# Kernel optimization log

Hardware: AMD Instinct MI355X
Metric: run time of the kernel (lower is better)

## Reference

```python
import jax, jax.numpy as jnp
import numpy as np
import math

H, W = 2048, 2048
Q_QUALITY = 50


def _dct_matrix():
    A = np.zeros((8, 8), dtype=np.float32)
    for i in range(8):
        for j in range(8):
            a = math.sqrt(1 / 8) if i == 0 else math.sqrt(1 / 4)
            A[i, j] = a * math.cos(math.pi * (j + 0.5) * i / 8)
    return A

_A = jnp.array(_dct_matrix())
_Qc = jnp.array([[17,18,24,47,99,99,99,99],[18,21,26,66,99,99,99,99],[24,26,56,99,99,99,99,99],[47,66,99,99,99,99,99,99],[99,99,99,99,99,99,99,99],[99,99,99,99,99,99,99,99],[99,99,99,99,99,99,99,99],[99,99,99,99,99,99,99,99]], dtype=jnp.float32)
_Qy = jnp.array([[16,11,10,16,24,40,51,61],[12,12,14,19,26,58,60,55],[14,13,16,24,40,57,69,56],[14,17,22,29,51,87,80,62],[18,22,37,56,68,109,103,77],[24,35,55,64,81,104,113,92],[49,64,78,87,103,121,120,101],[72,92,95,98,112,100,103,99]], dtype=jnp.float32)
_b = jnp.array([[0.0],[128.0],[128.0]], dtype=jnp.float32)
_w = jnp.array([[0.299,0.587,0.114],[-0.168736,-0.331264,0.5],[0.5,-0.418688,-0.081312]], dtype=jnp.float32)
_mean = jnp.array([125.3,123.0,113.9], dtype=jnp.float32) / 255.0
_std = jnp.array([63.0,62.1,66.7], dtype=jnp.float32) / 255.0


def setup_inputs() -> dict:
    key = jax.random.key(0)
    inp = jax.random.uniform(key, (1, 3, H, W), dtype=jnp.float32, minval=0.0, maxval=255.0)
    return {"input": inp}


def reference(input):
    img = input[0]                         # (3, H, W)
    C, h, w_ = img.shape
    # RGB -> YUV
    YUV = (_w @ img.reshape(3, -1) + _b).reshape(3, h, w_)
    # JPEG quality scale
    s = (50.0 / Q_QUALITY) if Q_QUALITY < 50 else (2.0 - 2.0 * Q_QUALITY / 100.0)
    Q = jnp.stack([_Qy * s, _Qc * s, _Qc * s])          # (3, 8, 8)
    Qb = Q[:, None, None]                                # (3, 1, 1, 8, 8)
    # blockize: (3, nH, nW, 8, 8)
    blocks = YUV.reshape(3, h // 8, 8, w_ // 8, 8).transpose(0, 1, 3, 2, 4)
    # blockwise DCT: A @ B @ A^T, then quantize
    dct = jnp.einsum('ij,chwjk,lk->chwil', _A, blocks, _A) / Qb
    r = jnp.round(dct)
    qd = r + (dct - r) ** 3                              # cubic rounding correction
    # dequantize + blockwise IDCT: A^T @ B @ A
    rec = jnp.einsum('ji,chwjk,kl->chwil', _A, qd * Qb, _A)
    iYUV = rec.transpose(0, 1, 3, 2, 4).reshape(3, h, w_)
    # YUV -> RGB
    rgb = (jnp.linalg.inv(_w) @ (iYUV.reshape(3, -1) - _b)).reshape(3, h, w_)
    # my_trans: normalize(pic / 255); model = identity -> flatten
    out = (rgb / 255.0 - _mean[:, None, None]) / _std[:, None, None]
    return out.reshape(1, -1)
```

## Files before the change

kernel.cpp:

```cpp
#include <hip/hip_runtime.h>
#include <math.h>

#define HH 2048
#define WW 2048
#define HWP (HH*WW)
#define NBLK 64
#define SLOTH 72

typedef _Float16 h8 __attribute__((ext_vector_type(8)));

#define C1d 0.49039264020161522
#define C2d 0.46193976625564337
#define C3d 0.41573480615127262
#define C4d 0.35355339059327379
#define C5d 0.27778511650980111
#define C6d 0.19134171618254489
#define C7d 0.097545161008064134
#define F(x) ((float)(x))

static constexpr float AFc[8][8] = {
 { F(C4d), F(C4d), F(C4d), F(C4d), F(C4d), F(C4d), F(C4d), F(C4d)},
 { F(C1d), F(C3d), F(C5d), F(C7d),-F(C7d),-F(C5d),-F(C3d),-F(C1d)},
 { F(C2d), F(C6d),-F(C6d),-F(C2d),-F(C2d),-F(C6d), F(C6d), F(C2d)},
 { F(C3d),-F(C7d),-F(C1d),-F(C5d), F(C5d), F(C1d), F(C7d),-F(C3d)},
 { F(C4d),-F(C4d),-F(C4d), F(C4d), F(C4d),-F(C4d),-F(C4d), F(C4d)},
 { F(C5d),-F(C1d), F(C7d), F(C3d),-F(C3d),-F(C7d), F(C1d),-F(C5d)},
 { F(C6d),-F(C2d), F(C2d),-F(C6d),-F(C6d), F(C2d),-F(C2d), F(C6d)},
 { F(C7d),-F(C5d), F(C3d),-F(C1d), F(C1d),-F(C3d), F(C5d),-F(C7d)}
};

__device__ __constant__ float g_AF[64] = {
  F(C4d), F(C4d), F(C4d), F(C4d), F(C4d), F(C4d), F(C4d), F(C4d),
  F(C1d), F(C3d), F(C5d), F(C7d),-F(C7d),-F(C5d),-F(C3d),-F(C1d),
  F(C2d), F(C6d),-F(C6d),-F(C2d),-F(C2d),-F(C6d), F(C6d), F(C2d),
  F(C3d),-F(C7d),-F(C1d),-F(C5d), F(C5d), F(C1d), F(C7d),-F(C3d),
  F(C4d),-F(C4d),-F(C4d), F(C4d), F(C4d),-F(C4d),-F(C4d), F(C4d),
  F(C5d),-F(C1d), F(C7d), F(C3d),-F(C3d),-F(C7d), F(C1d),-F(C5d),
  F(C6d),-F(C2d), F(C2d),-F(C6d),-F(C6d), F(C2d),-F(C2d), F(C6d),
  F(C7d),-F(C5d), F(C3d),-F(C1d), F(C1d),-F(C3d), F(C5d),-F(C7d)
};

__device__ __constant__ float g_Q[128] = {
 16,11,10,16,24,40,51,61,  12,12,14,19,26,58,60,55,
 14,13,16,24,40,57,69,56,  14,17,22,29,51,87,80,62,
 18,22,37,56,68,109,103,77, 24,35,55,64,81,104,113,92,
 49,64,78,87,103,121,120,101, 72,92,95,98,112,100,103,99,
 17,18,24,47,99,99,99,99,  18,21,26,66,99,99,99,99,
 24,26,56,99,99,99,99,99,  47,66,99,99,99,99,99,99,
 99,99,99,99,99,99,99,99,  99,99,99,99,99,99,99,99,
 99,99,99,99,99,99,99,99,  99,99,99,99,99,99,99,99};

static constexpr double W00=(double)0.299f,     W01=(double)0.587f,     W02=(double)0.114f;
static constexpr double W10=(double)-0.168736f, W11=(double)-0.331264f, W12=(double)0.5f;
static constexpr double W20=(double)0.5f,       W21=(double)-0.418688f, W22=(double)-0.081312f;
static constexpr double DETW = W00*(W11*W22 - W12*W21) - W01*(W10*W22 - W12*W20)
                             + W02*(W10*W21 - W11*W20);
static constexpr double I00=(W11*W22-W12*W21)/DETW, I01=(W02*W21-W01*W22)/DETW, I02=(W01*W12-W02*W11)/DETW;
static constexpr double I10=(W12*W20-W10*W22)/DETW, I11=(W00*W22-W02*W20)/DETW, I12=(W02*W10-W00*W12)/DETW;
static constexpr double I20=(W10*W21-W11*W20)/DETW, I21=(W01*W20-W00*W21)/DETW, I22=(W00*W11-W01*W10)/DETW;
static constexpr float  m0f = 125.3f/255.0f, m1f = 123.0f/255.0f, m2f = 113.9f/255.0f;
static constexpr float  s0f = 63.0f/255.0f,  s1f = 62.1f/255.0f,  s2f = 66.7f/255.0f;
static constexpr double M0d = 255.0*(double)m0f, M1d = 255.0*(double)m1f, M2d = 255.0*(double)m2f;
static constexpr double iS0d = 1.0/(255.0*(double)s0f), iS1d = 1.0/(255.0*(double)s1f), iS2d = 1.0/(255.0*(double)s2f);

__global__ void __launch_bounds__(192, 3)
jpeg_kernel(const float* __restrict__ in, float* __restrict__ out) {
#pragma clang fp contract(off)
  __shared__ _Float16 recs[3 * NBLK * SLOTH];
  __shared__ float Alds[64];
  __shared__ float Qlds[128];

  const int tid  = threadIdx.x;
  const int gid  = blockIdx.x;
  const int brow = gid >> 2;
  const int strip = gid & 3;
  const int rowbase = brow * 8;
  const int colbase = strip * 512;
  const int c   = tid >> 6;
  const int blk = tid & 63;

  if (tid < 64)        Alds[tid] = g_AF[tid];
  else if (tid < 192)  Qlds[tid - 64] = g_Q[tid - 64];
  __syncthreads();

  const float* pR = in;
  const float* pG = in + HWP;
  const float* pB = in + 2 * HWP;
  const size_t base = (size_t)rowbase * WW + colbase + blk * 8;

  float wc0, wc1, wc2, bc;
  if (c == 0)      { wc0 = 0.299f;     wc1 = 0.587f;     wc2 = 0.114f;     bc = 0.0f;   }
  else if (c == 1) { wc0 = -0.168736f; wc1 = -0.331264f; wc2 = 0.5f;       bc = 128.0f; }
  else             { wc0 = 0.5f;       wc1 = -0.418688f; wc2 = -0.081312f; bc = 128.0f; }

  float X[64];
  #pragma unroll
  for (int r = 0; r < 8; ++r) {
    const float* rowR = pR + base + (size_t)r * WW;
    const float* rowG = pG + base + (size_t)r * WW;
    const float* rowB = pB + base + (size_t)r * WW;
    float4 R0 = *(const float4*)rowR, R1 = *(const float4*)(rowR + 4);
    float4 G0 = *(const float4*)rowG, G1 = *(const float4*)(rowG + 4);
    float4 B0 = *(const float4*)rowB, B1 = *(const float4*)(rowB + 4);
    float fr[8] = {R0.x,R0.y,R0.z,R0.w,R1.x,R1.y,R1.z,R1.w};
    float fg[8] = {G0.x,G0.y,G0.z,G0.w,G1.x,G1.y,G1.z,G1.w};
    float fb[8] = {B0.x,B0.y,B0.z,B0.w,B1.x,B1.y,B1.z,B1.w};
    #pragma unroll
    for (int p = 0; p < 8; ++p) {
      float acc = fmaf(wc2, fb[p], fmaf(wc1, fg[p], wc0 * fr[p]));
      X[r*8+p] = acc + bc;
    }
  }

  _Float16* slot = recs + (c * NBLK + blk) * SLOTH;
  const float* Qrow = Qlds + ((c == 0) ? 0 : 64);
  for (int i = 0; i < 8; ++i) {
    float accs[8] = {0.f,0.f,0.f,0.f,0.f,0.f,0.f,0.f};
    #pragma unroll
    for (int j = 0; j < 8; ++j) {
      const float aij = Alds[i*8 + j];
      float P[8];
      #pragma unroll
      for (int k = 0; k < 8; ++k) P[k] = aij * X[j*8 + k];
      #pragma unroll
      for (int l = 0; l < 8; ++l) {
        #pragma unroll
        for (int k = 0; k < 8; ++k)
          accs[l] = accs[l] + P[k] * AFc[l][k];
      }
    }
    h8 rowv;
    #pragma unroll
    for (int l = 0; l < 8; ++l) {
      const float q  = Qrow[i*8 + l];
      const float v  = accs[l] / q;
      const float rr = rintf(v);
      const float e  = v - rr;
      const float qd = rr + (e * e) * e;
      rowv[l] = (_Float16)(qd * q);
    }
    *(h8*)(slot + i*8) = rowv;
  }

  float U[64];
  #pragma unroll
  for (int rw = 0; rw < 8; ++rw) {
    h8 v = *(const h8*)(slot + rw*8);
    #pragma unroll
    for (int k = 0; k < 8; ++k) U[rw*8+k] = (float)v[k];
  }
  #pragma unroll
  for (int j = 0; j < 8; ++j) {
    float t[8];
    #pragma unroll
    for (int n = 0; n < 8; ++n) {
      float acc = U[j*8+0] * AFc[0][n];
      #pragma unroll
      for (int k = 1; k < 8; ++k) acc = fmaf(U[j*8+k], AFc[k][n], acc);
      t[n] = acc;
    }
    #pragma unroll
    for (int n = 0; n < 8; ++n) U[j*8+n] = t[n];
  }
  #pragma unroll
  for (int n = 0; n < 8; ++n) {
    float t[8];
    #pragma unroll
    for (int m = 0; m < 8; ++m) {
      float acc = AFc[0][m] * U[0*8+n];
      #pragma unroll
      for (int j = 1; j < 8; ++j) acc = fmaf(AFc[j][m], U[j*8+n], acc);
      t[m] = acc;
    }
    #pragma unroll
    for (int m = 0; m < 8; ++m) U[m*8+n] = t[m];
  }
  #pragma unroll
  for (int rw = 0; rw < 8; ++rw) {
    h8 v;
    #pragma unroll
    for (int k = 0; k < 8; ++k) v[k] = (_Float16)U[rw*8+k];
    *(h8*)(slot + rw*8) = v;
  }
  __syncthreads();

  const float i00=F(I00), i01=F(I01), i02=F(I02);
  const float i10=F(I10), i11=F(I11), i12=F(I12);
  const float i20=F(I20), i21=F(I21), i22=F(I22);
  const float M0=F(M0d), M1=F(M1d), M2=F(M2d);
  const float iS0=F(iS0d), iS1=F(iS1d), iS2=F(iS2d);
  for (int g = tid; g < 512; g += 192) {
    const int b = g & 63;
    const int r = g >> 6;
    const h8 Yv = *(const h8*)(recs + (0*NBLK + b)*SLOTH + r*8);
    const h8 Uv = *(const h8*)(recs + (1*NBLK + b)*SLOTH + r*8);
    const h8 Vv = *(const h8*)(recs + (2*NBLK + b)*SLOTH + r*8);
    float o0[8], o1[8], o2[8];
    #pragma unroll
    for (int p = 0; p < 8; ++p) {
      const float yy = (float)Yv[p];
      const float uu = (float)Uv[p] - 128.0f;
      const float vv = (float)Vv[p] - 128.0f;
      o0[p] = (fmaf(i02, vv, fmaf(i01, uu, i00*yy)) - M0) * iS0;
      o1[p] = (fmaf(i12, vv, fmaf(i11, uu, i10*yy)) - M1) * iS1;
      o2[p] = (fmaf(i22, vv, fmaf(i21, uu, i20*yy)) - M2) * iS2;
    }
    const size_t off = (size_t)(rowbase + r) * WW + colbase + b * 8;
    *(float4*)(out + off)             = make_float4(o0[0],o0[1],o0[2],o0[3]);
    *(float4*)(out + off + 4)         = make_float4(o0[4],o0[5],o0[6],o0[7]);
    *(float4*)(out + HWP + off)       = make_float4(o1[0],o1[1],o1[2],o1[3]);
    *(float4*)(out + HWP + off + 4)   = make_float4(o1[4],o1[5],o1[6],o1[7]);
    *(float4*)(out + 2*HWP + off)     = make_float4(o2[0],o2[1],o2[2],o2[3]);
    *(float4*)(out + 2*HWP + off + 4) = make_float4(o2[4],o2[5],o2[6],o2[7]);
  }
}

extern "C" void kernel_launch(void* const* d_in, const int* in_sizes, int n_in,
                              void* d_out, int out_size, void* d_ws, size_t ws_size,
                              hipStream_t stream) {
  const float* in = (const float*)d_in[0];
  float* out = (float*)d_out;
  dim3 grid((HH/8) * (WW/512));
  dim3 block(192);
  jpeg_kernel<<<grid, block, 0, stream>>>(in, out);
}
```

Measured before the change: 130.2 us.

## Split each 8x8 block across two threads with packed f32x2 DCT math

```diff
diff --git a/kernel.cpp b/kernel.cpp
--- a/kernel.cpp
+++ b/kernel.cpp
@@ -4,10 +4,11 @@
 #define HH 2048
 #define WW 2048
 #define HWP (HH*WW)
-#define NBLK 64
+#define NBLK 32
 #define SLOTH 72
 
-typedef _Float16 h8 __attribute__((ext_vector_type(8)));
+typedef float     f2 __attribute__((ext_vector_type(2)));
+typedef _Float16  h8 __attribute__((ext_vector_type(8)));
 
 #define C1d 0.49039264020161522
 #define C2d 0.46193976625564337
@@ -63,21 +64,24 @@
 static constexpr double M0d = 255.0*(double)m0f, M1d = 255.0*(double)m1f, M2d = 255.0*(double)m2f;
 static constexpr double iS0d = 1.0/(255.0*(double)s0f), iS1d = 1.0/(255.0*(double)s1f), iS2d = 1.0/(255.0*(double)s2f);
 
-__global__ void __launch_bounds__(192, 3)
+__global__ void __launch_bounds__(192, 4)
 jpeg_kernel(const float* __restrict__ in, float* __restrict__ out) {
 #pragma clang fp contract(off)
-  __shared__ _Float16 recs[3 * NBLK * SLOTH];
+  __shared__ _Float16 buf[3 * NBLK * SLOTH];
   __shared__ float Alds[64];
   __shared__ float Qlds[128];
 
   const int tid  = threadIdx.x;
   const int gid  = blockIdx.x;
-  const int brow = gid >> 2;
-  const int strip = gid & 3;
+  const int brow = gid >> 3;
+  const int qcol = gid & 7;
   const int rowbase = brow * 8;
-  const int colbase = strip * 512;
+  const int colbase = qcol * 256;
   const int c   = tid >> 6;
-  const int blk = tid & 63;
+  const int sub = tid & 63;
+  const int blk = sub & 31;
+  const int h   = sub >> 5;
+  const int i0  = h * 4;
 
   if (tid < 64)        Alds[tid] = g_AF[tid];
   else if (tid < 192)  Qlds[tid - 64] = g_Q[tid - 64];
@@ -111,77 +115,89 @@
       X[r*8+p] = acc + bc;
     }
   }
-
-  _Float16* slot = recs + (c * NBLK + blk) * SLOTH;
-  const float* Qrow = Qlds + ((c == 0) ? 0 : 64);
-  for (int i = 0; i < 8; ++i) {
-    float accs[8] = {0.f,0.f,0.f,0.f,0.f,0.f,0.f,0.f};
+  const f2* X2 = (const f2*)X;
+
+  _Float16* slot = buf + (c * NBLK + blk) * SLOTH;
+  const int qoff = (c == 0) ? 0 : 64;
+
+  for (int ii = 0; ii < 4; ++ii) {
+    const int i = i0 + ii;
+    f2 accs2[4] = {(f2)0.f, (f2)0.f, (f2)0.f, (f2)0.f};
     #pragma unroll
     for (int j = 0; j < 8; ++j) {
       const float aij = Alds[i*8 + j];
-      float P[8];
-      #pragma unroll
-      for (int k = 0; k < 8; ++k) P[k] = aij * X[j*8 + k];
-      #pragma unroll
-      for (int l = 0; l < 8; ++l) {
+      const f2 av = (f2)aij;
+      f2 P2[4];
+      #pragma unroll
+      for (int kp = 0; kp < 4; ++kp) P2[kp] = av * X2[j*4 + kp];
+      const float* Pp = (const float*)P2;
+      #pragma unroll
+      for (int lp = 0; lp < 4; ++lp) {
         #pragma unroll
-        for (int k = 0; k < 8; ++k)
-          accs[l] = accs[l] + P[k] * AFc[l][k];
+        for (int k = 0; k < 8; ++k) {
+          const f2 ap = {AFc[2*lp][k], AFc[2*lp+1][k]};
+          f2 t = (f2)Pp[k] * ap;
+          accs2[lp] = accs2[lp] + t;
+        }
       }
     }
-    h8 rowv;
+    const float* ac = (const float*)accs2;
+    float Urow[8];
     #pragma unroll
     for (int l = 0; l < 8; ++l) {
-      const float q  = Qrow[i*8 + l];
-      const float v  = accs[l] / q;
+      const float q  = Qlds[qoff + i*8 + l];
+      const float v  = ac[l] / q;
       const float rr = rintf(v);
       const float e  = v - rr;
-      const float qd = rr + (e * e) * e;
-      rowv[l] = (_Float16)(qd * q);
-    }
-    *(h8*)(slot + i*8) = rowv;
-  }
-
-  float U[64];
-  #pragma unroll
-  for (int rw = 0; rw < 8; ++rw) {
-    h8 v = *(const h8*)(slot + rw*8);
-    #pragma unroll
-    for (int k = 0; k < 8; ++k) U[rw*8+k] = (float)v[k];
-  }
-  #pragma unroll
-  for (int j = 0; j < 8; ++j) {
-    float t[8];
-    #pragma unroll
-    for (int n = 0; n < 8; ++n) {
-      float acc = U[j*8+0] * AFc[0][n];
-      #pragma unroll
-      for (int k = 1; k < 8; ++k) acc = fmaf(U[j*8+k], AFc[k][n], acc);
-      t[n] = acc;
-    }
-    #pragma unroll
-    for (int n = 0; n < 8; ++n) U[j*8+n] = t[n];
-  }
-  #pragma unroll
-  for (int n = 0; n < 8; ++n) {
-    float t[8];
-    #pragma unroll
-    for (int m = 0; m < 8; ++m) {
-      float acc = AFc[0][m] * U[0*8+n];
-      #pragma unroll
-      for (int j = 1; j < 8; ++j) acc = fmaf(AFc[j][m], U[j*8+n], acc);
-      t[m] = acc;
-    }
-    #pragma unroll
-    for (int m = 0; m < 8; ++m) U[m*8+n] = t[m];
-  }
-  #pragma unroll
-  for (int rw = 0; rw < 8; ++rw) {
-    h8 v;
-    #pragma unroll
-    for (int k = 0; k < 8; ++k) v[k] = (_Float16)U[rw*8+k];
-    *(h8*)(slot + rw*8) = v;
-  }
+      Urow[l] = (rr + (e * e) * e) * q;
+    }
+    f2 vr[4] = {(f2)0.f, (f2)0.f, (f2)0.f, (f2)0.f};
+    #pragma unroll
+    for (int k = 0; k < 8; ++k) {
+      const f2 uk = (f2)Urow[k];
+      #pragma unroll
+      for (int np = 0; np < 4; ++np) {
+        const f2 ar = {AFc[k][2*np], AFc[k][2*np+1]};
+        vr[np] = __builtin_elementwise_fma(uk, ar, vr[np]);
+      }
+    }
+    h8 vh;
+    const float* vf = (const float*)vr;
+    #pragma unroll
+    for (int n = 0; n < 8; ++n) vh[n] = (_Float16)vf[n];
+    *(h8*)(slot + i*8) = vh;
+  }
+
+  h8 Vr[8];
+  #pragma unroll
+  for (int j = 0; j < 8; ++j) Vr[j] = *(const h8*)(slot + j*8);
+  float Vf[64];
+  #pragma unroll
+  for (int j = 0; j < 8; ++j)
+    #pragma unroll
+    for (int n = 0; n < 8; ++n) Vf[j*8+n] = (float)Vr[j][n];
+  const f2* Vf2 = (const f2*)Vf;
+
+  h8 rech[4];
+  #pragma unroll
+  for (int mm = 0; mm < 4; ++mm) {
+    const int m = i0 + mm;
+    f2 acc[4] = {(f2)0.f, (f2)0.f, (f2)0.f, (f2)0.f};
+    #pragma unroll
+    for (int j = 0; j < 8; ++j) {
+      const f2 ajm = (f2)Alds[j*8 + m];
+      #pragma unroll
+      for (int np = 0; np < 4; ++np)
+        acc[np] = __builtin_elementwise_fma(ajm, Vf2[j*4 + np], acc[np]);
+    }
+    const float* rf = (const float*)acc;
+    #pragma unroll
+    for (int n = 0; n < 8; ++n) rech[mm][n] = (_Float16)rf[n];
+  }
+  #pragma unroll
+  for (int mm = 0; mm < 4; ++mm)
+    *(h8*)(slot + (i0 + mm)*8) = rech[mm];
+
   __syncthreads();
 
   const float i00=F(I00), i01=F(I01), i02=F(I02);
@@ -189,12 +205,12 @@
   const float i20=F(I20), i21=F(I21), i22=F(I22);
   const float M0=F(M0d), M1=F(M1d), M2=F(M2d);
   const float iS0=F(iS0d), iS1=F(iS1d), iS2=F(iS2d);
-  for (int g = tid; g < 512; g += 192) {
-    const int b = g & 63;
-    const int r = g >> 6;
-    const h8 Yv = *(const h8*)(recs + (0*NBLK + b)*SLOTH + r*8);
-    const h8 Uv = *(const h8*)(recs + (1*NBLK + b)*SLOTH + r*8);
-    const h8 Vv = *(const h8*)(recs + (2*NBLK + b)*SLOTH + r*8);
+  for (int g = tid; g < 256; g += 192) {
+    const int b = g & 31;
+    const int r = g >> 5;
+    const h8 Yv = *(const h8*)(buf + (0*NBLK + b)*SLOTH + r*8);
+    const h8 Uv = *(const h8*)(buf + (1*NBLK + b)*SLOTH + r*8);
+    const h8 Vv = *(const h8*)(buf + (2*NBLK + b)*SLOTH + r*8);
     float o0[8], o1[8], o2[8];
     #pragma unroll
     for (int p = 0; p < 8; ++p) {
@@ -220,7 +236,7 @@
                               hipStream_t stream) {
   const float* in = (const float*)d_in[0];
   float* out = (float*)d_out;
-  dim3 grid((HH/8) * (WW/512));
+  dim3 grid((HH/8) * (WW/256));
   dim3 block(192);
   jpeg_kernel<<<grid, block, 0, stream>>>(in, out);
 }
```

After: 131.1 us. About the same (+0.7%).

## Stream input rows into forward DCT and keep quantized coefficients in registers

Applied to the files above, without the earlier changes.

```diff
diff --git a/kernel.cpp b/kernel.cpp
--- a/kernel.cpp
+++ b/kernel.cpp
@@ -7,7 +7,7 @@
 #define NBLK 64
 #define SLOTH 72
 
-typedef _Float16 h8 __attribute__((ext_vector_type(8)));
+typedef _Float16  h8 __attribute__((ext_vector_type(8)));
 
 #define C1d 0.49039264020161522
 #define C2d 0.46193976625564337
@@ -63,7 +63,7 @@
 static constexpr double M0d = 255.0*(double)m0f, M1d = 255.0*(double)m1f, M2d = 255.0*(double)m2f;
 static constexpr double iS0d = 1.0/(255.0*(double)s0f), iS1d = 1.0/(255.0*(double)s1f), iS2d = 1.0/(255.0*(double)s2f);
 
-__global__ void __launch_bounds__(192, 3)
+__global__ void __launch_bounds__(192, 4)
 jpeg_kernel(const float* __restrict__ in, float* __restrict__ out) {
 #pragma clang fp contract(off)
   __shared__ _Float16 recs[3 * NBLK * SLOTH];
@@ -93,94 +93,83 @@
   else if (c == 1) { wc0 = -0.168736f; wc1 = -0.331264f; wc2 = 0.5f;       bc = 128.0f; }
   else             { wc0 = 0.5f;       wc1 = -0.418688f; wc2 = -0.081312f; bc = 128.0f; }
 
-  float X[64];
-  #pragma unroll
-  for (int r = 0; r < 8; ++r) {
-    const float* rowR = pR + base + (size_t)r * WW;
-    const float* rowG = pG + base + (size_t)r * WW;
-    const float* rowB = pB + base + (size_t)r * WW;
-    float4 R0 = *(const float4*)rowR, R1 = *(const float4*)(rowR + 4);
-    float4 G0 = *(const float4*)rowG, G1 = *(const float4*)(rowG + 4);
-    float4 B0 = *(const float4*)rowB, B1 = *(const float4*)(rowB + 4);
-    float fr[8] = {R0.x,R0.y,R0.z,R0.w,R1.x,R1.y,R1.z,R1.w};
-    float fg[8] = {G0.x,G0.y,G0.z,G0.w,G1.x,G1.y,G1.z,G1.w};
-    float fb[8] = {B0.x,B0.y,B0.z,B0.w,B1.x,B1.y,B1.z,B1.w};
+  float accs[64];
+  #pragma unroll
+  for (int t = 0; t < 64; ++t) accs[t] = 0.0f;
+
+  float4 Ra = *(const float4*)(pR + base),         Rb = *(const float4*)(pR + base + 4);
+  float4 Ga = *(const float4*)(pG + base),         Gb = *(const float4*)(pG + base + 4);
+  float4 Ba = *(const float4*)(pB + base),         Bb = *(const float4*)(pB + base + 4);
+
+  for (int j = 0; j < 8; ++j) {
+    const float fr[8] = {Ra.x,Ra.y,Ra.z,Ra.w,Rb.x,Rb.y,Rb.z,Rb.w};
+    const float fg[8] = {Ga.x,Ga.y,Ga.z,Ga.w,Gb.x,Gb.y,Gb.z,Gb.w};
+    const float fb[8] = {Ba.x,Ba.y,Ba.z,Ba.w,Bb.x,Bb.y,Bb.z,Bb.w};
+    if (j < 7) {
+      const size_t nb = base + (size_t)(j + 1) * WW;
+      Ra = *(const float4*)(pR + nb); Rb = *(const float4*)(pR + nb + 4);
+      Ga = *(const float4*)(pG + nb); Gb = *(const float4*)(pG + nb + 4);
+      Ba = *(const float4*)(pB + nb); Bb = *(const float4*)(pB + nb + 4);
+    }
+    float Xj[8];
     #pragma unroll
     for (int p = 0; p < 8; ++p) {
       float acc = fmaf(wc2, fb[p], fmaf(wc1, fg[p], wc0 * fr[p]));
-      X[r*8+p] = acc + bc;
-    }
-  }
-
-  _Float16* slot = recs + (c * NBLK + blk) * SLOTH;
-  const float* Qrow = Qlds + ((c == 0) ? 0 : 64);
-  for (int i = 0; i < 8; ++i) {
-    float accs[8] = {0.f,0.f,0.f,0.f,0.f,0.f,0.f,0.f};
-    #pragma unroll
-    for (int j = 0; j < 8; ++j) {
+      Xj[p] = acc + bc;
+    }
+    #pragma unroll
+    for (int i = 0; i < 8; ++i) {
       const float aij = Alds[i*8 + j];
       float P[8];
       #pragma unroll
-      for (int k = 0; k < 8; ++k) P[k] = aij * X[j*8 + k];
+      for (int k = 0; k < 8; ++k) P[k] = aij * Xj[k];
       #pragma unroll
       for (int l = 0; l < 8; ++l) {
         #pragma unroll
         for (int k = 0; k < 8; ++k)
-          accs[l] = accs[l] + P[k] * AFc[l][k];
+          accs[i*8+l] = accs[i*8+l] + P[k] * AFc[l][k];
       }
     }
-    h8 rowv;
+  }
+
+  const int qoff = (c == 0) ? 0 : 64;
+  #pragma unroll
+  for (int i = 0; i < 8; ++i) {
     #pragma unroll
     for (int l = 0; l < 8; ++l) {
-      const float q  = Qrow[i*8 + l];
-      const float v  = accs[l] / q;
+      const float q  = Qlds[qoff + i*8 + l];
+      const float v  = accs[i*8+l] / q;
       const float rr = rintf(v);
       const float e  = v - rr;
-      const float qd = rr + (e * e) * e;
-      rowv[l] = (_Float16)(qd * q);
-    }
-    *(h8*)(slot + i*8) = rowv;
-  }
-
-  float U[64];
-  #pragma unroll
-  for (int rw = 0; rw < 8; ++rw) {
-    h8 v = *(const h8*)(slot + rw*8);
-    #pragma unroll
-    for (int k = 0; k < 8; ++k) U[rw*8+k] = (float)v[k];
-  }
-  #pragma unroll
-  for (int j = 0; j < 8; ++j) {
+      accs[i*8+l] = (rr + (e * e) * e) * q;
+    }
+  }
+
+  #pragma unroll
+  for (int i = 0; i < 8; ++i) {
     float t[8];
     #pragma unroll
     for (int n = 0; n < 8; ++n) {
-      float acc = U[j*8+0] * AFc[0][n];
-      #pragma unroll
-      for (int k = 1; k < 8; ++k) acc = fmaf(U[j*8+k], AFc[k][n], acc);
-      t[n] = acc;
-    }
-    #pragma unroll
-    for (int n = 0; n < 8; ++n) U[j*8+n] = t[n];
-  }
-  #pragma unroll
-  for (int n = 0; n < 8; ++n) {
-    float t[8];
-    #pragma unroll
-    for (int m = 0; m < 8; ++m) {
-      float acc = AFc[0][m] * U[0*8+n];
-      #pragma unroll
-      for (int j = 1; j < 8; ++j) acc = fmaf(AFc[j][m], U[j*8+n], acc);
-      t[m] = acc;
-    }
-    #pragma unroll
-    for (int m = 0; m < 8; ++m) U[m*8+n] = t[m];
-  }
-  #pragma unroll
-  for (int rw = 0; rw < 8; ++rw) {
-    h8 v;
-    #pragma unroll
-    for (int k = 0; k < 8; ++k) v[k] = (_Float16)U[rw*8+k];
-    *(h8*)(slot + rw*8) = v;
+      float a = accs[i*8+0] * AFc[0][n];
+      #pragma unroll
+      for (int k = 1; k < 8; ++k) a = fmaf(accs[i*8+k], AFc[k][n], a);
+      t[n] = a;
+    }
+    #pragma unroll
+    for (int n = 0; n < 8; ++n) accs[i*8+n] = t[n];
+  }
+  _Float16* slot = recs + (c * NBLK + blk) * SLOTH;
+  #pragma unroll
+  for (int m = 0; m < 8; ++m) {
+    h8 rh;
+    #pragma unroll
+    for (int n = 0; n < 8; ++n) {
+      float a = AFc[0][m] * accs[0*8+n];
+      #pragma unroll
+      for (int j = 1; j < 8; ++j) a = fmaf(AFc[j][m], accs[j*8+n], a);
+      rh[n] = (_Float16)a;
+    }
+    *(h8*)(slot + m*8) = rh;
   }
   __syncthreads();
 
```

Measured after the change: 142.2 us. 1.09x slower.
